# Performance work log

Hardware: AMD Instinct MI355X
Metric: run time of the kernel (lower is better)

The kernel has to match this reference:

```python
import jax, jax.numpy as jnp
import numpy as np
from jax import lax

NPG = 61      # nodes (electrodes) per graph, hard-coded by 61*hidden reshape
B = 128       # graphs per batch
L = 160       # raw signal length -> final conv length 1
NF = 64       # num_features
HC = 128      # hidden_channels
NCLS = 4


def setup_inputs() -> dict:
    key = jax.random.key(0)
    ks = jax.random.split(key, 16)
    N = B * NPG
    # fully-connected (no self-loops) edges within each graph -> 3660 edges/graph
    a = np.repeat(np.arange(NPG), NPG)
    b = np.tile(np.arange(NPG), NPG)
    m = a != b
    sl, dl = a[m], b[m]
    off = (np.arange(B) * NPG)[:, None]
    edge_index = np.stack([(sl[None] + off).ravel(), (dl[None] + off).ravel()]).astype(np.int64)
    batch = np.repeat(np.arange(B), NPG).astype(np.int64)

    def rn(k, shape, fan_in):
        return jax.random.normal(k, shape, jnp.float32) / np.sqrt(fan_in).astype(np.float32)

    return dict(
        x=jax.random.normal(ks[0], (N, L), jnp.float32),
        edge_index=jnp.asarray(edge_index),
        batch=jnp.asarray(batch),
        edge_features=jax.random.normal(ks[1], (edge_index.shape[1], 3), jnp.float32),
        conv_w0=rn(ks[2], (NF, 1, 7), 7.0), conv_b0=jnp.zeros((NF,), jnp.float32),
        conv_w1=rn(ks[3], (NF, NF, 5), NF * 5.0), conv_b1=jnp.zeros((NF,), jnp.float32),
        conv_w2=rn(ks[4], (NF, NF, 3), NF * 3.0), conv_b2=jnp.zeros((NF,), jnp.float32),
        bn1_g=jnp.ones((NF,), jnp.float32), bn1_b=jnp.zeros((NF,), jnp.float32),
        g_w0=rn(ks[5], (NF, HC), float(NF)), g_b0=jnp.zeros((HC,), jnp.float32),
        g_w1=rn(ks[6], (HC, HC), float(HC)), g_b1=jnp.zeros((HC,), jnp.float32),
        g_w2=rn(ks[7], (HC, HC), float(HC)), g_b2=jnp.zeros((HC,), jnp.float32),
        bn2_g=jnp.ones((HC,), jnp.float32), bn2_b=jnp.zeros((HC,), jnp.float32),
        lin_w0=rn(ks[8], (NPG * HC, HC), float(NPG * HC)), lin_b0=jnp.zeros((HC,), jnp.float32),
        lin_w1=rn(ks[9], (HC, HC), float(HC)), lin_b1=jnp.zeros((HC,), jnp.float32),
        lin_w2=rn(ks[10], (HC, NCLS), float(HC)), lin_b2=jnp.zeros((NCLS,), jnp.float32),
        edge_w=rn(ks[11], (3, 1), 3.0), edge_b=jnp.zeros((1,), jnp.float32),
    )


def _conv1d(x, w, b, pad):
    # x: [N, Cin, L], w: [Cout, Cin, K]
    y = lax.conv_general_dilated(x, w, (1,), [(pad, pad)], dimension_numbers=('NCH', 'OIH', 'NCH'))
    return y + b[None, :, None]


def _maxpool7(x):
    n = x.shape[-1] // 7
    return x[..., : n * 7].reshape(x.shape[0], x.shape[1], n, 7).max(-1)


def _bn(x, g, b):
    # BatchNorm1d in training mode: biased batch statistics
    m = x.mean(0)
    v = x.var(0)
    return (x - m) * lax.rsqrt(v + 1e-5) * g + b


def _forward(x, edge_features, conv_w0, conv_b0, conv_w1, conv_b1, conv_w2, conv_b2,
             bn1_g, bn1_b, g_w0, g_b0, g_w1, g_b1, g_w2, g_b2, bn2_g, bn2_b,
             lin_w0, lin_b0, lin_w1, lin_b1, lin_w2, lin_b2, edge_w, edge_b,
             edge_index, batch):
    N = x.shape[0]
    nb = N // NPG  # == batch.max()+1 for contiguous graph layout
    # tanh-gated edge weights
    ew = jnp.tanh(edge_features @ edge_w + edge_b)            # [E, 1]
    # Conv1d feature extractor: [N,1,160] -> [N,NF,1]
    h = x[:, None, :]
    h = _maxpool7(jax.nn.relu(_conv1d(h, conv_w0, conv_b0, 0)))   # [N,NF,22]
    h = jax.nn.relu(_conv1d(h, conv_w1, conv_b1, 2))               # [N,NF,22]
    h = _maxpool7(h)                                               # [N,NF,3]
    h = _conv1d(h, conv_w2, conv_b2, 0)[:, :, 0]                   # [N,NF]
    h = _bn(h, bn1_g, bn1_b)
    # Edge-weighted GCN hops (MyzConv): lin -> gather src -> scale -> scatter-add dst
    src, dst = edge_index[0], edge_index[1]
    for w, bs, act in ((g_w0, g_b0, True), (g_w1, g_b1, True), (g_w2, g_b2, False)):
        hw = h @ w + bs                                            # [N,HC]
        msg = ew * hw[src]                                         # [E,HC]
        h = jax.ops.segment_sum(msg, dst, num_segments=N)
        if act:
            h = jax.nn.relu(h)
    h = _bn(h, bn2_g, bn2_b)
    # MLP classifier over concatenated node features per graph
    h = h.reshape(nb, NPG * HC)
    h = jax.nn.relu(h @ lin_w0 + lin_b0)
    h = jax.nn.relu(h @ lin_w1 + lin_b1)
    h = h @ lin_w2 + lin_b2
    return jax.nn.log_softmax(h, -1), ew.reshape(nb, -1).T


def reference(x, edge_index, batch, edge_features, conv_w0, conv_b0, conv_w1, conv_b1,
              conv_w2, conv_b2, bn1_g, bn1_b, g_w0, g_b0, g_w1, g_b1, g_w2, g_b2,
              bn2_g, bn2_b, lin_w0, lin_b0, lin_w1, lin_b1, lin_w2, lin_b2, edge_w, edge_b):
    return _forward(x, edge_features, conv_w0, conv_b0, conv_w1, conv_b1, conv_w2, conv_b2,
                    bn1_g, bn1_b, g_w0, g_b0, g_w1, g_b1, g_w2, g_b2, bn2_g, bn2_b,
                    lin_w0, lin_b0, lin_w1, lin_b1, lin_w2, lin_b2, edge_w, edge_b,
                    edge_index, batch)
```

## Files before the change

### kernel.cpp

```cpp
#include <hip/hip_runtime.h>
#include <math.h>

#define NPGN 61
#define NGRAPH 128
#define NNODES (NPGN*NGRAPH)
#define EPG 3660

typedef float float4v __attribute__((ext_vector_type(4)));
typedef short bf16x8 __attribute__((ext_vector_type(8)));
typedef unsigned short u16;

__device__ __forceinline__ u16 f2bf(float v){
  union { float f; unsigned u; } x; x.f = v;
  unsigned r = (x.u + 0x7FFFu + ((x.u >> 16) & 1u)) >> 16;
  return (u16)r;
}
__device__ __forceinline__ float bf2f(unsigned u){
  union { unsigned u; float f; } x; x.u = u << 16;
  return x.f;
}

__global__ __launch_bounds__(256) void k_prep(const float* __restrict__ w0,
    const float* __restrict__ w1, const float* __restrict__ w2,
    const float* __restrict__ gw0, const float* __restrict__ gw1, const float* __restrict__ gw2,
    const float* __restrict__ lw0,
    float* __restrict__ w0t, u16* __restrict__ w1b, u16* __restrict__ w2b,
    u16* __restrict__ gwt0, u16* __restrict__ gwt1, u16* __restrict__ gwt2,
    u16* __restrict__ lw0t){
  __shared__ __align__(16) u16 tile[32*132];
  int b = blockIdx.x, tid = threadIdx.x;
  if (b < 290){
    int idx = b*256 + tid;
    if (idx < 20480){
      int f = idx / 320, r = idx - f*320;
      int kk = r >> 6, c = r & 63;
      w1b[idx] = f2bf(w1[f*320 + c*5 + kk]);
    } else if (idx < 32768){
      int j = idx - 20480; w2b[j] = f2bf(w2[j]);
    } else if (idx < 40960){
      int j = idx - 32768; int jj = j >> 6, k = j & 63; gwt0[j] = f2bf(gw0[k*128 + jj]);
    } else if (idx < 57344){
      int j = idx - 40960; int jj = j >> 7, k = j & 127; gwt1[j] = f2bf(gw1[k*128 + jj]);
    } else if (idx < 73728){
      int j = idx - 57344; int jj = j >> 7, k = j & 127; gwt2[j] = f2bf(gw2[k*128 + jj]);
    } else if (idx < 74176){
      int j = idx - 73728; int k = j >> 6, f = j & 63; w0t[j] = w0[f*7 + k];
    }
  } else {
    int bb = b - 290;
    int i = bb >> 2, oq = bb & 3;
    for (int idx = tid; idx < 4096; idx += 256){
      int k = idx >> 5, ol = idx & 31;
      tile[ol*132 + k] = f2bf(lw0[((size_t)i*128 + k)*128 + oq*32 + ol]);
    }
    __syncthreads();
    unsigned* dst = (unsigned*)lw0t;
    for (int idx = tid; idx < 2048; idx += 256){
      int ol = idx >> 6, kw = idx & 63;
      unsigned v = (unsigned)tile[ol*132 + 2*kw] | ((unsigned)tile[ol*132 + 2*kw + 1] << 16);
      dst[((size_t)i*128 + oq*32 + ol)*64 + kw] = v;
    }
  }
}

#define A0T_STR 72
#define C1_STR 24
#define NB 4
__global__ __launch_bounds__(256) void k_conv(const float* __restrict__ x,
    const float* __restrict__ w0t, const float* __restrict__ b0,
    const u16* __restrict__ w1b, const float* __restrict__ b1,
    const u16* __restrict__ w2b, const float* __restrict__ b2,
    float* __restrict__ h0, float* __restrict__ stat1p){
  int w = threadIdx.x >> 6, lane = threadIdx.x & 63;
  int tid = threadIdx.x;
  int q = lane >> 4, r16 = lane & 15;
  __shared__ __align__(16) float xs[NB][160];
  __shared__ __align__(16) u16 a0t[NB][36*A0T_STR];
  __shared__ __align__(16) u16 c1s[NB][64*C1_STR];
  __shared__ __align__(16) u16 a1k[NB][208];

  {
    const float* xb = x + (size_t)blockIdx.x*NB*160;
    float* xsf = &xs[0][0];
    #pragma unroll
    for (int idx = tid; idx < NB*160; idx += 256) xsf[idx] = xb[idx];
  }

  bf16x8 wf1[10], wf2[6];
  #pragma unroll
  for (int ks = 0; ks < 10; ks++)
    wf1[ks] = *(const bf16x8*)(w1b + (16*w + r16)*320 + ks*32 + q*8);
  #pragma unroll
  for (int ks = 0; ks < 6; ks++)
    wf2[ks] = *(const bf16x8*)(w2b + (16*w + r16)*192 + ks*32 + q*8);
  float4 b1v = *(const float4*)(b1 + 16*w + 4*q);
  float4 b2v = *(const float4*)(b2 + 16*w + 4*q);

  float w0r[7];
  #pragma unroll
  for (int k = 0; k < 7; k++) w0r[k] = w0t[k*64 + lane];
  float b0f = b0[lane];

  #pragma unroll
  for (int i2 = 0; i2 < 6; i2++){
    int rp = (i2 < 2) ? i2 : 22 + i2;
    a0t[w][rp*A0T_STR + lane] = 0;
  }
  __syncthreads();

  for (int j = w; j < 44; j += 4){
    int n = j / 11, qp = j - n*11;
    const float* xsp = &xs[n][0];
    float win[20];
    #pragma unroll
    for (int jj = 0; jj < 20; jj++) win[jj] = xsp[14*qp + jj];
    float m0, m1;
    #pragma unroll
    for (int r = 0; r < 7; r++){
      float s = w0r[0]*win[r];
      #pragma unroll
      for (int k = 1; k < 7; k++) s += w0r[k]*win[r+k];
      m0 = r ? fmaxf(m0, s) : s;
    }
    #pragma unroll
    for (int r = 7; r < 14; r++){
      float s = w0r[0]*win[r];
      #pragma unroll
      for (int k = 1; k < 7; k++) s += w0r[k]*win[r+k];
      m1 = (r > 7) ? fmaxf(m1, s) : s;
    }
    a0t[n][(2 + 2*qp)*A0T_STR + lane] = f2bf(fmaxf(m0 + b0f, 0.f));
    a0t[n][(3 + 2*qp)*A0T_STR + lane] = f2bf(fmaxf(m1 + b0f, 0.f));
  }
  __syncthreads();

  #pragma unroll 1
  for (int n = 0; n < NB; n++){
    float4v acc0 = {0.f,0.f,0.f,0.f}, acc1 = {0.f,0.f,0.f,0.f};
    #pragma unroll
    for (int ks = 0; ks < 10; ks++){
      int kk = ks >> 1;
      int cbase = (ks & 1)*32 + q*8;
      bf16x8 bv0 = *(const bf16x8*)(&a0t[n][(r16 + kk)*A0T_STR + cbase]);
      bf16x8 bv1 = *(const bf16x8*)(&a0t[n][(r16 + 16 + kk)*A0T_STR + cbase]);
      acc0 = __builtin_amdgcn_mfma_f32_16x16x32_bf16(wf1[ks], bv0, acc0, 0, 0, 0);
      acc1 = __builtin_amdgcn_mfma_f32_16x16x32_bf16(wf1[ks], bv1, acc1, 0, 0, 0);
    }
    #pragma unroll
    for (int reg = 0; reg < 4; reg++){
      int m = 16*w + q*4 + reg;
      float bv_ = ((const float*)&b1v)[reg];
      c1s[n][m*C1_STR + r16] = f2bf(fmaxf(acc0[reg] + bv_, 0.f));
      if (r16 <= 4)
        c1s[n][m*C1_STR + 16 + r16] = f2bf(fmaxf(acc1[reg] + bv_, 0.f));
    }
  }
  __syncthreads();

  {
    const u16* c1 = &c1s[w][0];
    bf16x8 f0 = *(const bf16x8*)(c1 + lane*C1_STR);
    bf16x8 f1 = *(const bf16x8*)(c1 + lane*C1_STR + 8);
    bf16x8 f2 = *(const bf16x8*)(c1 + lane*C1_STR + 16);
    float v[24];
    #pragma unroll
    for (int j = 0; j < 8; j++){
      v[j]    = bf2f((u16)f0[j]);
      v[8+j]  = bf2f((u16)f1[j]);
      v[16+j] = bf2f((u16)f2[j]);
    }
    #pragma unroll
    for (int t = 0; t < 3; t++){
      float m = v[t*7];
      #pragma unroll
      for (int r = 1; r < 7; r++) m = fmaxf(m, v[t*7+r]);
      a1k[w][lane*3 + t] = f2bf(m);
    }
  }
  __syncthreads();

  float4v sacc = {0.f,0.f,0.f,0.f}, qacc = {0.f,0.f,0.f,0.f};
  #pragma unroll 1
  for (int n = 0; n < NB; n++){
    float4v acc2 = {0.f,0.f,0.f,0.f};
    #pragma unroll
    for (int ks = 0; ks < 6; ks++){
      bf16x8 bs = *(const bf16x8*)(&a1k[n][ks*32 + q*8]);
      acc2 = __builtin_amdgcn_mfma_f32_16x16x32_bf16(wf2[ks], bs, acc2, 0, 0, 0);
    }
    if (r16 == 0){
      int nn = blockIdx.x*NB + n;
      #pragma unroll
      for (int reg = 0; reg < 4; reg++){
        int f = 16*w + 4*q + reg;
        float v = acc2[reg] + ((const float*)&b2v)[reg];
        h0[(size_t)nn*64 + f] = v;
        sacc[reg] += v;
        qacc[reg] += v*v;
      }
    }
  }

  if (r16 == 0){
    int bkt = blockIdx.x & 31;
    #pragma unroll
    for (int reg = 0; reg < 4; reg++){
      int f = 16*w + 4*q + reg;
      atomicAdd(&stat1p[bkt*128 + f], sacc[reg]);
      atomicAdd(&stat1p[bkt*128 + 64 + f], qacc[reg]);
    }
  }
}

#define EW_STR 72
#define HS_STR 136
#define HWT_STR 72
__global__ __launch_bounds__(512) void k_gnn(const float* __restrict__ h0,
    const float* __restrict__ stat1p,
    const float* __restrict__ bn1g, const float* __restrict__ bn1b,
    const u16* __restrict__ gwt0, const float* __restrict__ gb0,
    const u16* __restrict__ gwt1, const float* __restrict__ gb1,
    const u16* __restrict__ gwt2, const float* __restrict__ gb2,
    const float* __restrict__ ef, const float* __restrict__ eww,
    const float* __restrict__ ewb, float* __restrict__ out2,
    u16* __restrict__ hB, float* __restrict__ stat2p){
  int g = blockIdx.x, tid = threadIdx.x;
  int w = tid >> 6, lane = tid & 63, q = lane >> 4, r16 = lane & 15;
  int dt = w & 3, jh = w >> 2;
  __shared__ u16 hs[64*HS_STR];
  __shared__ u16 hwT[128*HWT_STR];
  __shared__ u16 ewl[64*EW_STR];
  __shared__ float bsc[64], bsh[64];
  __shared__ float st2[256];

  bf16x8 af0[2], af1[4], af2[4];
  #pragma unroll
  for (int ks = 0; ks < 2; ks++)
    af0[ks] = *(const bf16x8*)(gwt0 + (16*w + r16)*64 + ks*32 + q*8);
  #pragma unroll
  for (int ks = 0; ks < 4; ks++)
    af1[ks] = *(const bf16x8*)(gwt1 + (16*w + r16)*128 + ks*32 + q*8);
  #pragma unroll
  for (int ks = 0; ks < 4; ks++)
    af2[ks] = *(const bf16x8*)(gwt2 + (16*w + r16)*128 + ks*32 + q*8);
  float4 b40 = *(const float4*)(gb0 + 16*w + 4*q);
  float4 b41 = *(const float4*)(gb1 + 16*w + 4*q);
  float4 b42 = *(const float4*)(gb2 + 16*w + 4*q);

  if (tid < 64){
    float s = 0.f, s2 = 0.f;
    #pragma unroll
    for (int r = 0; r < 32; r++){
      s  += stat1p[r*128 + tid];
      s2 += stat1p[r*128 + 64 + tid];
    }
    float m = s*(1.f/NNODES), v = s2*(1.f/NNODES) - m*m;
    float sc = rsqrtf(v + 1e-5f)*bn1g[tid];
    bsc[tid] = sc; bsh[tid] = bn1b[tid] - m*sc;
  }
  if (tid < 256) st2[tid] = 0.f;
  {
    unsigned* td = (unsigned*)ewl;
    for (int idx = tid; idx < 64*EW_STR/2; idx += 512) td[idx] = 0;
  }
  {
    unsigned* hsd = (unsigned*)hs;
    for (int idx = tid; idx < 3*(HS_STR/2); idx += 512){
      int rr = 61 + idx/(HS_STR/2), cc = idx%(HS_STR/2);
      hsd[rr*(HS_STR/2) + cc] = 0;
    }
  }
  __syncthreads();

  {
    float v0 = eww[0], v1 = eww[1], v2 = eww[2], bb = ewb[0];
    const float* efg = ef + (size_t)g*EPG*3;
    for (int idx = tid; idx < EPG; idx += 512){
      const float* p = efg + idx*3;
      float v = tanhf(p[0]*v0 + p[1]*v1 + p[2]*v2 + bb);
      int s = idx/60, r = idx - s*60;
      int d = r + (r >= s ? 1 : 0);
      ewl[d*EW_STR + s] = f2bf(v);
      out2[(size_t)idx*128 + g] = v;
    }
  }
  {
    unsigned* hsd = (unsigned*)hs;
    for (int idx = tid; idx < 61*32; idx += 512){
      int i = idx >> 5, kw = idx & 31;
      float2 hv = *(const float2*)(h0 + ((size_t)g*61 + i)*64 + kw*2);
      int k0 = kw*2;
      float a = hv.x*bsc[k0] + bsh[k0];
      float b = hv.y*bsc[k0+1] + bsh[k0+1];
      hsd[i*(HS_STR/2) + kw] = (unsigned)f2bf(a) | ((unsigned)f2bf(b) << 16);
    }
  }
  __syncthreads();
  bf16x8 ewf[2];
  #pragma unroll
  for (int ks = 0; ks < 2; ks++)
    ewf[ks] = *(const bf16x8*)(ewl + (16*dt + r16)*EW_STR + ks*32 + q*8);

  #pragma unroll
  for (int nt = 0; nt < 4; nt++){
    float4v acc = {b40.x, b40.y, b40.z, b40.w};
    #pragma unroll
    for (int ks = 0; ks < 2; ks++){
      bf16x8 bv = *(const bf16x8*)(hs + (nt*16 + r16)*HS_STR + ks*32 + q*8);
      acc = __builtin_amdgcn_mfma_f32_16x16x32_bf16(af0[ks], bv, acc, 0, 0, 0);
    }
    #pragma unroll
    for (int r = 0; r < 4; r++)
      hwT[(16*w + 4*q + r)*HWT_STR + nt*16 + r16] = f2bf(acc[r]);
  }
  __syncthreads();
  #pragma unroll
  for (int nt = 0; nt < 4; nt++){
    int j = (jh*4 + nt)*16;
    float4v acc = {0.f,0.f,0.f,0.f};
    #pragma unroll
    for (int ks = 0; ks < 2; ks++){
      bf16x8 bv = *(const bf16x8*)(hwT + (j + r16)*HWT_STR + ks*32 + q*8);
      acc = __builtin_amdgcn_mfma_f32_16x16x32_bf16(ewf[ks], bv, acc, 0, 0, 0);
    }
    #pragma unroll
    for (int r = 0; r < 4; r++){
      int d = 16*dt + 4*q + r;
      hs[d*HS_STR + j + r16] = f2bf(fmaxf(acc[r], 0.f));
    }
  }
  __syncthreads();

  #pragma unroll
  for (int nt = 0; nt < 4; nt++){
    float4v acc = {b41.x, b41.y, b41.z, b41.w};
    #pragma unroll
    for (int ks = 0; ks < 4; ks++){
      bf16x8 bv = *(const bf16x8*)(hs + (nt*16 + r16)*HS_STR + ks*32 + q*8);
      acc = __builtin_amdgcn_mfma_f32_16x16x32_bf16(af1[ks], bv, acc, 0, 0, 0);
    }
    #pragma unroll
    for (int r = 0; r < 4; r++)
      hwT[(16*w + 4*q + r)*HWT_STR + nt*16 + r16] = f2bf(acc[r]);
  }
  __syncthreads();
  #pragma unroll
  for (int nt = 0; nt < 4; nt++){
    int j = (jh*4 + nt)*16;
    float4v acc = {0.f,0.f,0.f,0.f};
    #pragma unroll
    for (int ks = 0; ks < 2; ks++){
      bf16x8 bv = *(const bf16x8*)(hwT + (j + r16)*HWT_STR + ks*32 + q*8);
      acc = __builtin_amdgcn_mfma_f32_16x16x32_bf16(ewf[ks], bv, acc, 0, 0, 0);
    }
    #pragma unroll
    for (int r = 0; r < 4; r++){
      int d = 16*dt + 4*q + r;
      hs[d*HS_STR + j + r16] = f2bf(fmaxf(acc[r], 0.f));
    }
  }
  __syncthreads();

  #pragma unroll
  for (int nt = 0; nt < 4; nt++){
    float4v acc = {b42.x, b42.y, b42.z, b42.w};
    #pragma unroll
    for (int ks = 0; ks < 4; ks++){
      bf16x8 bv = *(const bf16x8*)(hs + (nt*16 + r16)*HS_STR + ks*32 + q*8);
      acc = __builtin_amdgcn_mfma_f32_16x16x32_bf16(af2[ks], bv, acc, 0, 0, 0);
    }
    #pragma unroll
    for (int r = 0; r < 4; r++)
      hwT[(16*w + 4*q + r)*HWT_STR + nt*16 + r16] = f2bf(acc[r]);
  }
  __syncthreads();
  #pragma unroll
  for (int nt = 0; nt < 4; nt++){
    int j = (jh*4 + nt)*16;
    float4v acc = {0.f,0.f,0.f,0.f};
    #pragma unroll
    for (int ks = 0; ks < 2; ks++){
      bf16x8 bv = *(const bf16x8*)(hwT + (j + r16)*HWT_STR + ks*32 + q*8);
      acc = __builtin_amdgcn_mfma_f32_16x16x32_bf16(ewf[ks], bv, acc, 0, 0, 0);
    }
    float cs = 0.f, cq = 0.f;
    #pragma unroll
    for (int r = 0; r < 4; r++){
      int d = 16*dt + 4*q + r;
      if (d < 61){
        float v = acc[r];
        hB[((size_t)g*61 + d)*128 + j + r16] = f2bf(v);
        cs += v; cq += v*v;
      }
    }
    int col = j + r16;
    atomicAdd(&st2[col], cs);
    atomicAdd(&st2[128 + col], cq);
  }
  __syncthreads();
  if (tid < 256) stat2p[(size_t)tid*128 + g] = st2[tid];
}

#define AS_STR 136
__global__ __launch_bounds__(256) void k_mlp0(const u16* __restrict__ hB,
    const float* __restrict__ stat2p,
    const float* __restrict__ bn2g, const float* __restrict__ bn2b,
    const u16* __restrict__ lw0t, float* __restrict__ y0pre){
  int bi = blockIdx.x; int i = bi >> 2, sub = bi & 3;
  int oh = sub & 1, gh = sub >> 1;
  int tid = threadIdx.x, w = tid >> 6, lane = tid & 63, q = lane >> 4, r16 = lane & 15;
  __shared__ u16 As[64*AS_STR];
  __shared__ float sc2[128], sh2[128];
  if (tid < 128){
    float4v sa = {0,0,0,0}, sb = {0,0,0,0};
    #pragma unroll
    for (int r = 0; r < 32; r++){
      sa += *(const float4v*)(stat2p + (size_t)tid*128 + r*4);
      sb += *(const float4v*)(stat2p + (size_t)(128 + tid)*128 + r*4);
    }
    float s = sa[0]+sa[1]+sa[2]+sa[3], s2 = sb[0]+sb[1]+sb[2]+sb[3];
    float m = s*(1.f/NNODES), v = s2*(1.f/NNODES) - m*m;
    float sc = rsqrtf(v + 1e-5f)*bn2g[tid];
    sc2[tid] = sc; sh2[tid] = bn2b[tid] - m*sc;
  }
  __syncthreads();
  {
    const unsigned* hbd = (const unsigned*)hB;
    unsigned* asd = (unsigned*)As;
    for (int idx = tid; idx < 4096; idx += 256){
      int gg = gh*64 + (idx >> 6), kw = idx & 63;
      unsigned pv = hbd[((size_t)gg*61 + i)*64 + kw];
      int k0 = kw*2;
      float a = bf2f(pv & 0xffffu)*sc2[k0] + sh2[k0];
      float b = bf2f(pv >> 16)*sc2[k0+1] + sh2[k0+1];
      asd[(idx >> 6)*(AS_STR/2) + kw] = (unsigned)f2bf(a) | ((unsigned)f2bf(b) << 16);
    }
  }
  __syncthreads();
  const u16* wbase = lw0t + ((size_t)i*128 + oh*64)*128;
  bf16x8 af[4];
  #pragma unroll
  for (int ks = 0; ks < 4; ks++)
    af[ks] = *(const bf16x8*)(As + (16*w + r16)*AS_STR + ks*32 + q*8);
  #pragma unroll
  for (int nt = 0; nt < 4; nt++){
    float4v acc = {0.f,0.f,0.f,0.f};
    #pragma unroll
    for (int ks = 0; ks < 4; ks++){
      bf16x8 bv = *(const bf16x8*)(wbase + (size_t)(nt*16 + r16)*128 + ks*32 + q*8);
      acc = __builtin_amdgcn_mfma_f32_16x16x32_bf16(af[ks], bv, acc, 0, 0, 0);
    }
    #pragma unroll
    for (int r = 0; r < 4; r++){
      int g = gh*64 + 16*w + 4*q + r;
      atomicAdd(&y0pre[(size_t)g*128 + oh*64 + nt*16 + r16], acc[r]);
    }
  }
}

__global__ __launch_bounds__(128) void k_mlp1(const float* __restrict__ y0pre,
    const float* __restrict__ lb0, const float* __restrict__ W1,
    const float* __restrict__ lb1, const float* __restrict__ W2,
    const float* __restrict__ lb2, float* __restrict__ out){
  int g = blockIdx.x, o = threadIdx.x;
  __shared__ float y0[128], y1[128], red[128];
  y0[o] = fmaxf(y0pre[(size_t)g*128 + o] + lb0[o], 0.f);
  __syncthreads();
  float a = lb1[o];
  #pragma unroll 8
  for (int k = 0; k < 128; k++) a += y0[k]*W1[k*128 + o];
  y1[o] = fmaxf(a, 0.f);
  __syncthreads();
  int c = o & 3, kb = o >> 2;
  float a2 = 0.f;
  #pragma unroll
  for (int j = 0; j < 4; j++){
    int k = kb + 32*j;
    a2 += y1[k]*W2[k*4 + c];
  }
  red[o] = a2;
  __syncthreads();
  #pragma unroll
  for (int off = 64; off >= 4; off >>= 1){
    if (o < off) red[o] += red[o + off];
    __syncthreads();
  }
  if (o == 0){
    float v0 = red[0]+lb2[0], v1 = red[1]+lb2[1], v2 = red[2]+lb2[2], v3 = red[3]+lb2[3];
    float m = fmaxf(fmaxf(v0,v1), fmaxf(v2,v3));
    float lse = m + logf(expf(v0-m)+expf(v1-m)+expf(v2-m)+expf(v3-m));
    out[g*4+0]=v0-lse; out[g*4+1]=v1-lse; out[g*4+2]=v2-lse; out[g*4+3]=v3-lse;
  }
}

extern "C" void kernel_launch(void* const* d_in, const int* in_sizes, int n_in,
                              void* d_out, int out_size, void* d_ws, size_t ws_size,
                              hipStream_t stream){
  const float* x    = (const float*)d_in[0];
  const float* ef   = (const float*)d_in[3];
  const float* cw0  = (const float*)d_in[4];
  const float* cb0  = (const float*)d_in[5];
  const float* cw1  = (const float*)d_in[6];
  const float* cb1  = (const float*)d_in[7];
  const float* cw2  = (const float*)d_in[8];
  const float* cb2  = (const float*)d_in[9];
  const float* bn1g = (const float*)d_in[10];
  const float* bn1b = (const float*)d_in[11];
  const float* gw0  = (const float*)d_in[12];
  const float* gb0  = (const float*)d_in[13];
  const float* gw1  = (const float*)d_in[14];
  const float* gb1  = (const float*)d_in[15];
  const float* gw2  = (const float*)d_in[16];
  const float* gb2  = (const float*)d_in[17];
  const float* bn2g = (const float*)d_in[18];
  const float* bn2b = (const float*)d_in[19];
  const float* lw0  = (const float*)d_in[20];
  const float* lb0  = (const float*)d_in[21];
  const float* lw1  = (const float*)d_in[22];
  const float* lb1  = (const float*)d_in[23];
  const float* lw2  = (const float*)d_in[24];
  const float* lb2  = (const float*)d_in[25];
  const float* eww  = (const float*)d_in[26];
  const float* ewb  = (const float*)d_in[27];
  float* out = (float*)d_out;

  float* ws   = (float*)d_ws;
  float* w1s  = ws;
  float* w2s  = w1s + 10240;
  float* w0t  = w2s + 6144;
  float* gws0 = w0t + 448;
  float* gws1 = gws0 + 4096;
  float* gws2 = gws1 + 8192;
  float* h0   = gws2 + 8192;
  float* hBs  = h0 + 499712;
  float* lw0s = hBs + 499712;
  float* accs = lw0s + 499712;

  u16* w1b    = (u16*)w1s;
  u16* w2b    = (u16*)w2s;
  u16* gwt0   = (u16*)gws0;
  u16* gwt1   = (u16*)gws1;
  u16* gwt2   = (u16*)gws2;
  u16* hB     = (u16*)hBs;
  u16* lw0t   = (u16*)lw0s;
  float* stat1p = accs;
  float* y0pre  = accs + 4096;
  float* stat2p = accs + 20480;

  hipMemsetAsync(accs, 0, 20480*sizeof(float), stream);
  k_prep <<<534, 256, 0, stream>>>(cw0, cw1, cw2, gw0, gw1, gw2, lw0,
                                   w0t, w1b, w2b, gwt0, gwt1, gwt2, lw0t);
  k_conv <<<NNODES/NB, 256, 0, stream>>>(x, w0t, cb0, w1b, cb1, w2b, cb2, h0, stat1p);
  k_gnn  <<<NGRAPH, 512, 0, stream>>>(h0, stat1p, bn1g, bn1b,
                                      gwt0, gb0, gwt1, gb1, gwt2, gb2,
                                      ef, eww, ewb, out + 512, hB, stat2p);
  k_mlp0 <<<NPGN*4, 256, 0, stream>>>(hB, stat2p, bn2g, bn2b, lw0t, y0pre);
  k_mlp1 <<<NGRAPH, 128, 0, stream>>>(y0pre, lb0, lw1, lb1, lw2, lb2, out);
}
```

Before: 199.1 us.

## Move edge-weight computation into conv kernel and fold memset into prep

Edge-weight tanh computation and the out2 scatter move from the per-graph GNN kernel into extra blocks of the conv launch. Those blocks write a bf16 padded matrix per graph to a workspace that the GNN kernel loads directly into MFMA fragments, which frees GNN shared memory and a serial phase. The hipMemsetAsync of the accumulators is replaced by extra blocks in k_prep, removing one launch. The cost is an extra global round trip for the edge matrix and some extra blocks in the conv grid.

```diff
diff --git a/kernel.cpp b/kernel.cpp
--- a/kernel.cpp
+++ b/kernel.cpp
@@ -5,6 +5,7 @@
 #define NGRAPH 128
 #define NNODES (NPGN*NGRAPH)
 #define EPG 3660
+#define NCONVB (NNODES/4)
 
 typedef float float4v __attribute__((ext_vector_type(4)));
 typedef short bf16x8 __attribute__((ext_vector_type(8)));
@@ -26,9 +27,14 @@
     const float* __restrict__ lw0,
     float* __restrict__ w0t, u16* __restrict__ w1b, u16* __restrict__ w2b,
     u16* __restrict__ gwt0, u16* __restrict__ gwt1, u16* __restrict__ gwt2,
-    u16* __restrict__ lw0t){
+    u16* __restrict__ lw0t, float* __restrict__ accs){
   __shared__ __align__(16) u16 tile[32*132];
   int b = blockIdx.x, tid = threadIdx.x;
+  if (b >= 534){
+    int idx = (b - 534)*256 + tid;
+    if (idx < 20480) accs[idx] = 0.f;
+    return;
+  }
   if (b < 290){
     int idx = b*256 + tid;
     if (idx < 20480){
@@ -66,13 +72,35 @@
 #define A0T_STR 72
 #define C1_STR 24
 #define NB 4
+#define EW_STR 72
 __global__ __launch_bounds__(256) void k_conv(const float* __restrict__ x,
     const float* __restrict__ w0t, const float* __restrict__ b0,
     const u16* __restrict__ w1b, const float* __restrict__ b1,
     const u16* __restrict__ w2b, const float* __restrict__ b2,
-    float* __restrict__ h0, float* __restrict__ stat1p){
-  int w = threadIdx.x >> 6, lane = threadIdx.x & 63;
+    float* __restrict__ h0, float* __restrict__ stat1p,
+    const float* __restrict__ ef, const float* __restrict__ eww,
+    const float* __restrict__ ewb, float* __restrict__ out2,
+    u16* __restrict__ ews){
   int tid = threadIdx.x;
+  if (blockIdx.x >= NCONVB){
+    int g = blockIdx.x - NCONVB;
+    u16* eg = ews + (size_t)g*(64*EW_STR);
+    for (int idx = tid; idx < 64*EW_STR; idx += 256) eg[idx] = 0;
+    __syncthreads();
+    float v0 = eww[0], v1 = eww[1], v2 = eww[2], bb = ewb[0];
+    const float* efg = ef + (size_t)g*EPG*3;
+    for (int idx = tid; idx < EPG; idx += 256){
+      const float* p = efg + idx*3;
+      float v = tanhf(p[0]*v0 + p[1]*v1 + p[2]*v2 + bb);
+      int s = idx/60, r = idx - s*60;
+      int d = r + (r >= s ? 1 : 0);
+      eg[d*EW_STR + s] = f2bf(v);
+      out2[(size_t)idx*128 + g] = v;
+    }
+    return;
+  }
+
+  int w = tid >> 6, lane = tid & 63;
   int q = lane >> 4, r16 = lane & 15;
   __shared__ __align__(16) float xs[NB][160];
   __shared__ __align__(16) u16 a0t[NB][36*A0T_STR];
@@ -212,7 +240,6 @@
   }
 }
 
-#define EW_STR 72
 #define HS_STR 136
 #define HWT_STR 72
 __global__ __launch_bounds__(512) void k_gnn(const float* __restrict__ h0,
@@ -221,19 +248,17 @@
     const u16* __restrict__ gwt0, const float* __restrict__ gb0,
     const u16* __restrict__ gwt1, const float* __restrict__ gb1,
     const u16* __restrict__ gwt2, const float* __restrict__ gb2,
-    const float* __restrict__ ef, const float* __restrict__ eww,
-    const float* __restrict__ ewb, float* __restrict__ out2,
+    const u16* __restrict__ ews,
     u16* __restrict__ hB, float* __restrict__ stat2p){
   int g = blockIdx.x, tid = threadIdx.x;
   int w = tid >> 6, lane = tid & 63, q = lane >> 4, r16 = lane & 15;
   int dt = w & 3, jh = w >> 2;
   __shared__ u16 hs[64*HS_STR];
   __shared__ u16 hwT[128*HWT_STR];
-  __shared__ u16 ewl[64*EW_STR];
   __shared__ float bsc[64], bsh[64];
   __shared__ float st2[256];
 
-  bf16x8 af0[2], af1[4], af2[4];
+  bf16x8 af0[2], af1[4], af2[4], ewf[2];
   #pragma unroll
   for (int ks = 0; ks < 2; ks++)
     af0[ks] = *(const bf16x8*)(gwt0 + (16*w + r16)*64 + ks*32 + q*8);
@@ -243,6 +268,9 @@
   #pragma unroll
   for (int ks = 0; ks < 4; ks++)
     af2[ks] = *(const bf16x8*)(gwt2 + (16*w + r16)*128 + ks*32 + q*8);
+  #pragma unroll
+  for (int ks = 0; ks < 2; ks++)
+    ewf[ks] = *(const bf16x8*)(ews + (size_t)g*(64*EW_STR) + (16*dt + r16)*EW_STR + ks*32 + q*8);
   float4 b40 = *(const float4*)(gb0 + 16*w + 4*q);
   float4 b41 = *(const float4*)(gb1 + 16*w + 4*q);
   float4 b42 = *(const float4*)(gb2 + 16*w + 4*q);
@@ -259,10 +287,6 @@
     bsc[tid] = sc; bsh[tid] = bn1b[tid] - m*sc;
   }
   if (tid < 256) st2[tid] = 0.f;
-  {
-    unsigned* td = (unsigned*)ewl;
-    for (int idx = tid; idx < 64*EW_STR/2; idx += 512) td[idx] = 0;
-  }
   {
     unsigned* hsd = (unsigned*)hs;
     for (int idx = tid; idx < 3*(HS_STR/2); idx += 512){
@@ -272,18 +296,6 @@
   }
   __syncthreads();
 
-  {
-    float v0 = eww[0], v1 = eww[1], v2 = eww[2], bb = ewb[0];
-    const float* efg = ef + (size_t)g*EPG*3;
-    for (int idx = tid; idx < EPG; idx += 512){
-      const float* p = efg + idx*3;
-      float v = tanhf(p[0]*v0 + p[1]*v1 + p[2]*v2 + bb);
-      int s = idx/60, r = idx - s*60;
-      int d = r + (r >= s ? 1 : 0);
-      ewl[d*EW_STR + s] = f2bf(v);
-      out2[(size_t)idx*128 + g] = v;
-    }
-  }
   {
     unsigned* hsd = (unsigned*)hs;
     for (int idx = tid; idx < 61*32; idx += 512){
@@ -296,10 +308,6 @@
     }
   }
   __syncthreads();
-  bf16x8 ewf[2];
-  #pragma unroll
-  for (int ks = 0; ks < 2; ks++)
-    ewf[ks] = *(const bf16x8*)(ewl + (16*dt + r16)*EW_STR + ks*32 + q*8);
 
   #pragma unroll
   for (int nt = 0; nt < 4; nt++){
@@ -535,6 +543,7 @@
   float* hBs  = h0 + 499712;
   float* lw0s = hBs + 499712;
   float* accs = lw0s + 499712;
+  float* ewss = accs + 53248;
 
   u16* w1b    = (u16*)w1s;
   u16* w2b    = (u16*)w2s;
@@ -543,17 +552,19 @@
   u16* gwt2   = (u16*)gws2;
   u16* hB     = (u16*)hBs;
   u16* lw0t   = (u16*)lw0s;
+  u16* ews    = (u16*)ewss;
   float* stat1p = accs;
   float* y0pre  = accs + 4096;
   float* stat2p = accs + 20480;
 
-  hipMemsetAsync(accs, 0, 20480*sizeof(float), stream);
-  k_prep <<<534, 256, 0, stream>>>(cw0, cw1, cw2, gw0, gw1, gw2, lw0,
-                                   w0t, w1b, w2b, gwt0, gwt1, gwt2, lw0t);
-  k_conv <<<NNODES/NB, 256, 0, stream>>>(x, w0t, cb0, w1b, cb1, w2b, cb2, h0, stat1p);
+  k_prep <<<615, 256, 0, stream>>>(cw0, cw1, cw2, gw0, gw1, gw2, lw0,
+                                   w0t, w1b, w2b, gwt0, gwt1, gwt2, lw0t, accs);
+  k_conv <<<NCONVB + NGRAPH, 256, 0, stream>>>(x, w0t, cb0, w1b, cb1, w2b, cb2,
+                                               h0, stat1p, ef, eww, ewb,
+                                               out + 512, ews);
   k_gnn  <<<NGRAPH, 512, 0, stream>>>(h0, stat1p, bn1g, bn1b,
                                       gwt0, gb0, gwt1, gb1, gwt2, gb2,
-                                      ef, eww, ewb, out + 512, hB, stat2p);
+                                      ews, hB, stat2p);
   k_mlp0 <<<NPGN*4, 256, 0, stream>>>(hB, stat2p, bn2g, bn2b, lw0t, y0pre);
   k_mlp1 <<<NGRAPH, 128, 0, stream>>>(y0pre, lb0, lw1, lb1, lw2, lb2, out);
 }
```

After: 195.0 us. 1.02x faster.
